# Kernel optimization log

Hardware: AMD Instinct MI355X
Metric: run time of the kernel (lower is better)

The kernel has to match this reference:

```python
import jax, jax.numpy as jnp
import numpy as np

D = 64          # embedding_dim
NU = 100000     # num_users
NI = 50000      # num_items
N = NU + NI     # total nodes
B = 16384       # batch of (user,item) pairs
CF = 256        # content_feat_dim
E = 2000000     # interaction edges (self loops added in forward)


def setup_inputs() -> dict:
    key = jax.random.key(0)
    ks = jax.random.split(key, 20)
    s = 0.05
    return {
        "user_ids": jnp.arange(B, dtype=jnp.int32),
        "item_ids": jnp.arange(B, dtype=jnp.int32),
        "content_features": jax.random.normal(ks[0], (B, CF), jnp.float32),
        "edge_index": jax.random.randint(ks[1], (2, E), 0, N, jnp.int32),
        # embeddings / projections
        "user_emb_w": jax.random.normal(ks[2], (NU, D), jnp.float32) * s,
        "item_emb_w": jax.random.normal(ks[3], (NI, D), jnp.float32) * s,
        "cp_w": jax.random.normal(ks[4], (CF, D), jnp.float32) * s,
        "cp_b": jnp.zeros((D,), jnp.float32),
        # GATConv1: in 2D, out D, heads 2, concat -> out dim 2D
        "w1": jax.random.normal(ks[5], (2 * D, 2 * D), jnp.float32) * s,
        "asrc1": jax.random.normal(ks[6], (2, D), jnp.float32) * s,
        "adst1": jax.random.normal(ks[7], (2, D), jnp.float32) * s,
        "b1": jnp.zeros((2 * D,), jnp.float32),
        # GATConv2: in 2D, out D, heads 1
        "w2": jax.random.normal(ks[8], (2 * D, D), jnp.float32) * s,
        "asrc2": jax.random.normal(ks[9], (1, D), jnp.float32) * s,
        "adst2": jax.random.normal(ks[10], (1, D), jnp.float32) * s,
        "b2": jnp.zeros((D,), jnp.float32),
        # predict head: Linear(3D,D) -> ReLU -> Linear(D,1)
        "pw1": jax.random.normal(ks[11], (3 * D, D), jnp.float32) * s,
        "pb1": jnp.zeros((D,), jnp.float32),
        "pw2": jax.random.normal(ks[12], (D, 1), jnp.float32) * s,
        "pb2": jnp.zeros((1,), jnp.float32),
    }


def _gat(x, src, dst, W, a_src, a_dst, bias, heads, C):
    # x: [N, in]; W: [in, heads*C]; a_src/a_dst: [heads, C]
    xw = (x @ W).reshape(N, heads, C)                      # [N,H,C]
    al_s = (xw * a_src[None]).sum(-1)                      # [N,H]
    al_d = (xw * a_dst[None]).sum(-1)                      # [N,H]
    e = jax.nn.leaky_relu(al_s[src] + al_d[dst], 0.2)      # [Et,H]
    m = jax.ops.segment_max(e, dst, num_segments=N)        # segment softmax
    ex = jnp.exp(e - m[dst])
    den = jax.ops.segment_sum(ex, dst, num_segments=N)
    alpha = ex / (den[dst] + 1e-16)                        # [Et,H]
    msg = xw[src] * alpha[:, :, None]                      # [Et,H,C]
    out = jax.ops.segment_sum(msg, dst, num_segments=N)    # [N,H,C]
    return out.reshape(N, heads * C) + bias


def reference(user_ids, item_ids, content_features, edge_index,
              user_emb_w, item_emb_w, cp_w, cp_b,
              w1, asrc1, adst1, b1, w2, asrc2, adst2, b2,
              pw1, pb1, pw2, pb2):
    u_emb = user_emb_w[user_ids]                           # [B,D]
    i_emb = item_emb_w[item_ids]                           # [B,D]
    c_emb = content_features @ cp_w + cp_b                 # [B,D]

    x = jnp.zeros((N, 2 * D), dtype=u_emb.dtype)
    x = x.at[user_ids].set(jnp.concatenate([u_emb, jnp.zeros_like(c_emb)], 1))
    x = x.at[NU + item_ids].set(jnp.concatenate([i_emb, c_emb], 1))

    loop = jnp.arange(N, dtype=edge_index.dtype)           # add_self_loops
    src = jnp.concatenate([edge_index[0], loop])
    dst = jnp.concatenate([edge_index[1], loop])

    x = jax.nn.elu(_gat(x, src, dst, w1, asrc1, adst1, b1, 2, D))  # [N,2D]
    x = _gat(x, src, dst, w2, asrc2, adst2, b2, 1, D)              # [N,D]

    combined = jnp.concatenate([u_emb, x[NU + item_ids], x[user_ids]], 1)  # [B,3D]
    h = jax.nn.relu(combined @ pw1 + pb1)
    return (h @ pw2 + pb2).squeeze(-1)                     # [B]
```

## Files before the change

### kernel.cpp

```cpp
#include <hip/hip_runtime.h>
#include <hip/hip_fp16.h>
#include <math.h>

static constexpr int ND  = 150000;
static constexpr int NUU = 100000;
static constexpr int BB  = 16384;
static constexpr int EE  = 2000000;
static constexpr int ETOT = EE + ND;
static constexpr int MACT = 2 * BB;

static constexpr int NBUK  = (ND + 127) >> 7;
static constexpr int CAP   = 4096;
static constexpr int CHUNK = 4096;
static constexpr int NCH   = (ETOT + CHUNK - 1) / CHUNK;
static constexpr int NBMW  = (ND + 31) / 32;
static constexpr unsigned long long M21 = 0x1FFFFF;

typedef _Float16 h8 __attribute__((ext_vector_type(8)));
typedef float    f4 __attribute__((ext_vector_type(4)));

__device__ __forceinline__ float wsum64(float v){
#pragma unroll
  for (int d = 32; d > 0; d >>= 1) v += __shfl_xor(v, d, 64);
  return v;
}

__global__ __launch_bounds__(256) void k_prep(const float* __restrict__ content,
    const float* __restrict__ cpw, const float* __restrict__ cpb,
    float* __restrict__ cemb,
    const float* __restrict__ w1, const float* __restrict__ w2,
    __half* __restrict__ Wt1, __half* __restrict__ Wt2,
    const float* __restrict__ asrc1, const float* __restrict__ adst1,
    const float* __restrict__ asrc2, const float* __restrict__ adst2,
    float* __restrict__ wa1s, float* __restrict__ wa1d,
    float* __restrict__ wa2s, float* __restrict__ wa2d){
  __shared__ __align__(16) float As[64 * 68];
  __shared__ __align__(16) float Ws[64 * 68];
  int tid = threadIdx.x;
  if (blockIdx.x < 256) {
    int m_base = blockIdx.x * 64;
    int tm = (tid >> 4) * 4, tn = (tid & 15) * 4;
    int lm = tid >> 2, lq = tid & 3;
    float acc[4][4];
#pragma unroll
    for (int i = 0; i < 4; i++)
#pragma unroll
      for (int j = 0; j < 4; j++) acc[i][j] = 0.f;
    for (int ks = 0; ks < 256; ks += 64) {
#pragma unroll
      for (int p = 0; p < 4; p++) {
        float4 v = *(const float4*)(content + (size_t)(m_base + lm) * 256 + ks + lq * 16 + p * 4);
        *(float4*)(As + lm * 68 + lq * 16 + p * 4) = v;
      }
#pragma unroll
      for (int p = 0; p < 4; p++) {
        int n4 = lq + p * 4;
        float4 v = *(const float4*)(cpw + (size_t)(ks + lm) * 64 + n4 * 4);
        *(float4*)(Ws + lm * 68 + n4 * 4) = v;
      }
      __syncthreads();
#pragma unroll
      for (int kk = 0; kk < 64; kk += 4) {
        float4 a[4], wv[4];
#pragma unroll
        for (int i = 0; i < 4; i++) a[i] = *(const float4*)(As + (tm + i) * 68 + kk);
#pragma unroll
        for (int q = 0; q < 4; q++) wv[q] = *(const float4*)(Ws + (kk + q) * 68 + tn);
#pragma unroll
        for (int i = 0; i < 4; i++) {
          acc[i][0] = fmaf(a[i].x, wv[0].x, acc[i][0]); acc[i][1] = fmaf(a[i].x, wv[0].y, acc[i][1]);
          acc[i][2] = fmaf(a[i].x, wv[0].z, acc[i][2]); acc[i][3] = fmaf(a[i].x, wv[0].w, acc[i][3]);
          acc[i][0] = fmaf(a[i].y, wv[1].x, acc[i][0]); acc[i][1] = fmaf(a[i].y, wv[1].y, acc[i][1]);
          acc[i][2] = fmaf(a[i].y, wv[1].z, acc[i][2]); acc[i][3] = fmaf(a[i].y, wv[1].w, acc[i][3]);
          acc[i][0] = fmaf(a[i].z, wv[2].x, acc[i][0]); acc[i][1] = fmaf(a[i].z, wv[2].y, acc[i][1]);
          acc[i][2] = fmaf(a[i].z, wv[2].z, acc[i][2]); acc[i][3] = fmaf(a[i].z, wv[2].w, acc[i][3]);
          acc[i][0] = fmaf(a[i].w, wv[3].x, acc[i][0]); acc[i][1] = fmaf(a[i].w, wv[3].y, acc[i][1]);
          acc[i][2] = fmaf(a[i].w, wv[3].z, acc[i][2]); acc[i][3] = fmaf(a[i].w, wv[3].w, acc[i][3]);
        }
      }
      __syncthreads();
    }
    float4 bias = *(const float4*)(cpb + tn);
#pragma unroll
    for (int i = 0; i < 4; i++) {
      float4 o = make_float4(acc[i][0] + bias.x, acc[i][1] + bias.y,
                             acc[i][2] + bias.z, acc[i][3] + bias.w);
      *(float4*)(cemb + (size_t)(m_base + tm + i) * 64 + tn) = o;
    }
  } else if (blockIdx.x < 352) {
    int t = (blockIdx.x - 256) * 256 + tid;
    if (t < 16384) {
      int n = t >> 7, k = t & 127;
      Wt1[t] = __float2half(w1[k * 128 + n]);
    } else {
      int u = t - 16384;
      int n = u >> 7, k = u & 127;
      Wt2[u] = __float2half(w2[k * 64 + n]);
    }
  } else if (tid < 128) {
    int k = tid;
    float s0 = 0.f, s1 = 0.f, d0 = 0.f, d1 = 0.f, s2 = 0.f, d2 = 0.f;
    for (int c = 0; c < 64; c++) {
      float wA = w1[k * 128 + c];
      float wB = w1[k * 128 + 64 + c];
      s0 = fmaf(wA, asrc1[c], s0);       d0 = fmaf(wA, adst1[c], d0);
      s1 = fmaf(wB, asrc1[64 + c], s1);  d1 = fmaf(wB, adst1[64 + c], d1);
      float wC = w2[k * 64 + c];
      s2 = fmaf(wC, asrc2[c], s2);       d2 = fmaf(wC, adst2[c], d2);
    }
    wa1s[k * 2] = s0; wa1s[k * 2 + 1] = s1;
    wa1d[k * 2] = d0; wa1d[k * 2 + 1] = d1;
    wa2s[k] = s2; wa2d[k] = d2;
  }
}

__global__ __launch_bounds__(256) void k_scatter(const int* __restrict__ uids,
    const float* __restrict__ uemb, const float* __restrict__ cemb,
    const float* __restrict__ iemb, const int* __restrict__ iids,
    __half* __restrict__ xc,
    const float* __restrict__ wa1s, const float* __restrict__ wa1d,
    float* __restrict__ als1c, float* __restrict__ ald1,
    int* __restrict__ flags, unsigned* __restrict__ bitmap,
    int* __restrict__ nodeOfC){
  int t = blockIdx.x * 256 + threadIdx.x;
  int r = t >> 6, c = t & 63;
  float2 ws = *(const float2*)(wa1s + 2 * c);
  float2 wd = *(const float2*)(wa1d + 2 * c);
  if (r < BB) {
    int uid = uids[r];
    float u = uemb[(size_t)uid * 64 + c];
    xc[(size_t)r * 128 + c]      = __float2half(u);
    xc[(size_t)r * 128 + 64 + c] = __float2half(0.f);
    float s0 = wsum64(u * ws.x);
    float s1 = wsum64(u * ws.y);
    float d0 = wsum64(u * wd.x);
    float d1 = wsum64(u * wd.y);
    if (c == 0) {
      *(float2*)(als1c + (size_t)r * 2) = make_float2(s0, s1);
      *(float2*)(ald1 + (size_t)uid * 2) = make_float2(d0, d1);
      flags[uid] = r;
      nodeOfC[r] = uid;
      atomicOr(&bitmap[uid >> 5], 1u << (uid & 31));
    }
  } else {
    int b = r - BB;
    int iid = iids[b];
    int node = NUU + iid;
    float lo = iemb[(size_t)iid * 64 + c];
    float hi = cemb[(size_t)b * 64 + c];
    xc[(size_t)r * 128 + c]      = __float2half(lo);
    xc[(size_t)r * 128 + 64 + c] = __float2half(hi);
    float2 wsH = *(const float2*)(wa1s + 128 + 2 * c);
    float2 wdH = *(const float2*)(wa1d + 128 + 2 * c);
    float s0 = wsum64(lo * ws.x + hi * wsH.x);
    float s1 = wsum64(lo * ws.y + hi * wsH.y);
    float d0 = wsum64(lo * wd.x + hi * wdH.x);
    float d1 = wsum64(lo * wd.y + hi * wdH.y);
    if (c == 0) {
      *(float2*)(als1c + (size_t)r * 2) = make_float2(s0, s1);
      *(float2*)(ald1 + (size_t)node * 2) = make_float2(d0, d1);
      flags[node] = r;
      nodeOfC[r] = node;
      atomicOr(&bitmap[node >> 5], 1u << (node & 31));
    }
  }
}

__global__ __launch_bounds__(256) void k_bin(const int* __restrict__ ei,
    const unsigned* __restrict__ bitmap, unsigned long long* __restrict__ bcnt64,
    int* __restrict__ bdata){
  __shared__ unsigned long long h64[NBUK];
  __shared__ int base[NBUK];
  __shared__ int hist[NBUK];
  int tid = threadIdx.x;
  int t0 = blockIdx.x * CHUNK;
  for (int i = tid; i < NBUK; i += 256) h64[i] = 0ull;
  __syncthreads();
  for (int i = tid; i < CHUNK; i += 256) {
    int t = t0 + i;
    if (t >= ETOT) break;
    int src, dst;
    if (t < EE) { src = ei[t]; dst = ei[EE + t]; }
    else        { src = dst = t - EE; }
    unsigned long long sa = (bitmap[src >> 5] >> (src & 31)) & 1;
    unsigned long long da = (bitmap[dst >> 5] >> (dst & 31)) & 1;
    atomicAdd(&h64[dst >> 7], 1ull | (sa << 21) | (da << 42));
  }
  __syncthreads();
  for (int b = tid; b < NBUK; b += 256) {
    unsigned long long v = h64[b];
    base[b] = v ? (int)(atomicAdd(&bcnt64[b], v) & M21) : 0;
    hist[b] = 0;
  }
  __syncthreads();
  for (int i = tid; i < CHUNK; i += 256) {
    int t = t0 + i;
    if (t >= ETOT) break;
    int src, dst;
    if (t < EE) { src = ei[t]; dst = ei[EE + t]; }
    else        { src = dst = t - EE; }
    int sa = (bitmap[src >> 5] >> (src & 31)) & 1;
    int da = (bitmap[dst >> 5] >> (dst & 31)) & 1;
    int b = dst >> 7;
    int r = base[b] + atomicAdd(&hist[b], 1);
    if (r < CAP)
      bdata[(size_t)b * CAP + r] = src | (sa << 18) | (da << 19) | ((dst & 127) << 20);
  }
}

__global__ void k_bscan(const unsigned long long* __restrict__ bcnt64,
    int* __restrict__ bbaseA, int* __restrict__ bbaseB,
    int* __restrict__ offsA_end, int* __restrict__ csrA, int* __restrict__ csrB){
  int lane = threadIdx.x;
  int cA = 0, cB = 0;
  for (int c0 = 0; c0 < NBUK; c0 += 64) {
    int i = c0 + lane;
    unsigned long long v = (i < NBUK) ? bcnt64[i] : 0ull;
    int a = (int)((v >> 21) & M21);
    int b = (int)((v >> 42) & M21);
    int xa = a, xb = b;
#pragma unroll
    for (int d = 1; d < 64; d <<= 1) {
      int ta = __shfl_up(xa, d, 64); if (lane >= d) xa += ta;
      int tb = __shfl_up(xb, d, 64); if (lane >= d) xb += tb;
    }
    if (i < NBUK) { bbaseA[i] = cA + xa - a; bbaseB[i] = cB + xb - b; }
    cA += __shfl(xa, 63, 64);
    cB += __shfl(xb, 63, 64);
  }
  if (lane == 0) *offsA_end = cA;
  if (lane < 16) { csrA[cA + lane] = 0; csrB[cB + lane] = 0; }
}

__global__ __launch_bounds__(256) void k_bucket(const int* __restrict__ bdata,
    const unsigned long long* __restrict__ bcnt64,
    const int* __restrict__ bbaseA, const int* __restrict__ bbaseB,
    const int* __restrict__ flags,
    int* __restrict__ offsA, int* __restrict__ inactA,
    int* __restrict__ startB, int* __restrict__ degBv,
    int* __restrict__ csrA, int* __restrict__ csrB){
  __shared__ int degAll[128], degAct[128], curA[128], curB[128];
  int b = blockIdx.x;
  int tid = threadIdx.x;
  int cnt = (int)(bcnt64[b] & M21);
  const int* bd = bdata + (size_t)b * CAP;
  if (tid < 128) { degAll[tid] = 0; degAct[tid] = 0; }
  __syncthreads();
  for (int i = tid; i < cnt; i += 256) {
    int e = bd[i];
    int d7 = (e >> 20) & 127;
    atomicAdd(&degAll[d7], 1);
    if ((e >> 18) & 1) atomicAdd(&degAct[d7], 1);
  }
  __syncthreads();
  if (tid < 64) {
    int g0 = b * 128 + tid, g1 = g0 + 64;
    int A0 = degAll[tid], A1 = degAll[64 + tid];
    int a0 = degAct[tid], a1 = degAct[64 + tid];
    int s0 = a0, s1 = a1;
#pragma unroll
    for (int d = 1; d < 64; d <<= 1) {
      int t0 = __shfl_up(s0, d, 64); if (tid >= d) s0 += t0;
      int t1 = __shfl_up(s1, d, 64); if (tid >= d) s1 += t1;
    }
    int totA0 = __shfl(s0, 63, 64);
    int eA0 = s0 - a0, eA1 = s1 - a1 + totA0;
    int baseA = bbaseA[b];
    curA[tid] = baseA + eA0; curA[64 + tid] = baseA + eA1;
    if (g0 < ND) { offsA[g0] = baseA + eA0; inactA[g0] = A0 - a0; }
    if (g1 < ND) { offsA[g1] = baseA + eA1; inactA[g1] = A1 - a1; }
    int f0 = (g0 < ND) ? flags[g0] : -1;
    int f1 = (g1 < ND) ? flags[g1] : -1;
    int w0 = (f0 >= 0) ? A0 : 0, w1 = (f1 >= 0) ? A1 : 0;
    int t0 = w0, t1 = w1;
#pragma unroll
    for (int d = 1; d < 64; d <<= 1) {
      int u0 = __shfl_up(t0, d, 64); if (tid >= d) t0 += u0;
      int u1 = __shfl_up(t1, d, 64); if (tid >= d) t1 += u1;
    }
    int totB0 = __shfl(t0, 63, 64);
    int eB0 = t0 - w0, eB1 = t1 - w1 + totB0;
    int baseB = bbaseB[b];
    curB[tid] = baseB + eB0; curB[64 + tid] = baseB + eB1;
    if (f0 >= 0) { startB[f0] = baseB + eB0; degBv[f0] = A0; }
    if (f1 >= 0) { startB[f1] = baseB + eB1; degBv[f1] = A1; }
  }
  __syncthreads();
  for (int i = tid; i < cnt; i += 256) {
    int e = bd[i];
    int d7 = (e >> 20) & 127;
    int src = e & 0x3FFFF;
    if ((e >> 19) & 1) { int p = atomicAdd(&curB[d7], 1); csrB[p] = src; }
    if ((e >> 18) & 1) {
      int ci = flags[src];
      int p = atomicAdd(&curA[d7], 1);
      csrA[p] = ci;
    }
  }
}

template<int NT>
__global__ __launch_bounds__(256) void k_mfma(const __half* __restrict__ A,
    const __half* __restrict__ Bt, __half* __restrict__ C, int M){
  constexpr int N = NT * 16;
  int wid  = (blockIdx.x * 256 + threadIdx.x) >> 6;
  int lane = threadIdx.x & 63;
  int q = lane >> 4, mr = lane & 15;
  int r0 = wid * 32;
  if (r0 >= M) return;
  int row0 = min(r0 + mr, M - 1);
  int row1 = min(r0 + 16 + mr, M - 1);
  f4 acc[2][NT];
#pragma unroll
  for (int i = 0; i < 2; i++)
#pragma unroll
    for (int j = 0; j < NT; j++) acc[i][j] = (f4)0.f;
#pragma unroll
  for (int ks = 0; ks < 4; ks++) {
    int ko = ks * 32 + q * 8;
    h8 a0 = *(const h8*)(A + (size_t)row0 * 128 + ko);
    h8 a1 = *(const h8*)(A + (size_t)row1 * 128 + ko);
#pragma unroll
    for (int nt = 0; nt < NT; nt++) {
      h8 b = *(const h8*)(Bt + (size_t)(nt * 16 + mr) * 128 + ko);
      acc[0][nt] = __builtin_amdgcn_mfma_f32_16x16x32_f16(a0, b, acc[0][nt], 0, 0, 0);
      acc[1][nt] = __builtin_amdgcn_mfma_f32_16x16x32_f16(a1, b, acc[1][nt], 0, 0, 0);
    }
  }
#pragma unroll
  for (int mt = 0; mt < 2; mt++)
#pragma unroll
    for (int r = 0; r < 4; r++) {
      int row = r0 + mt * 16 + q * 4 + r;
      if (row < M) {
#pragma unroll
        for (int nt = 0; nt < NT; nt++)
          C[(size_t)row * N + nt * 16 + mr] = __float2half(acc[mt][nt][r]);
      }
    }
}

template<int U>
__device__ __forceinline__ void gat2_blk(const int* __restrict__ cp, int j0,
    const float* __restrict__ myp, const __half2* __restrict__ xw, int lane,
    float& accx, float& accy){
  __half2 hv[U]; float pj[U];
#pragma unroll
  for (int u = 0; u < U; u++) {
    int sj = __builtin_amdgcn_readfirstlane(cp[j0 + u]);
    hv[u] = xw[(size_t)sj * 64 + lane];
    pj[u] = myp[j0 + u];
  }
#pragma unroll
  for (int u = 0; u < U; u++) {
    float2 fv = __half22float2(hv[u]);
    accx = fmaf(pj[u], fv.x, accx);
    accy = fmaf(pj[u], fv.y, accy);
  }
}

template<int U>
__device__ __forceinline__ void gat1_blk(const int* __restrict__ cp, int j0,
    const float* __restrict__ myp, const __half2* __restrict__ xw, int cw, int hid,
    float& accx, float& accy){
  __half2 hv[U]; float pj[U];
#pragma unroll
  for (int u = 0; u < U; u++) {
    int j = j0 + 2 * u;
    int s0 = __builtin_amdgcn_readfirstlane(cp[j]);
    int s1 = __builtin_amdgcn_readfirstlane(cp[j + 1]);
    int sel = hid ? s1 : s0;
    hv[u] = xw[(size_t)sel * 32 + cw];
    pj[u] = myp[j];
  }
#pragma unroll
  for (int u = 0; u < U; u++) {
    float2 fv = __half22float2(hv[u]);
    accx = fmaf(pj[u], fv.x, accx);
    accy = fmaf(pj[u], fv.y, accy);
  }
}

__global__ __launch_bounds__(256) void k_agg2(const __half2* __restrict__ xwc,
    const float* __restrict__ als1c, const float* __restrict__ ald1,
    const int* __restrict__ offsA, const int* __restrict__ inactA,
    const int* __restrict__ csrA,
    const float* __restrict__ bias, __half* __restrict__ out,
    const float* __restrict__ wa2s, const float* __restrict__ wa2d,
    float* __restrict__ als2, float* __restrict__ ald2, int n){
  __shared__ float pshare[4][2][64];
  int gw = (blockIdx.x * 256 + threadIdx.x) >> 6;
  int lane = threadIdx.x & 63;
  int ws = (threadIdx.x >> 6) & 3;
  if (gw >= n) return;
  int e0 = __builtin_amdgcn_readfirstlane(offsA[gw]);
  int e1 = __builtin_amdgcn_readfirstlane(offsA[gw + 1]);
  int inact = __builtin_amdgcn_readfirstlane(inactA[gw]);
  float2 aldv = *(const float2*)(ald1 + (size_t)gw * 2);
  bool lo = lane < 32;
  const float* myp = &pshare[ws][0][0] + (lo ? 0 : 64);
  float den0 = 0.f, den1 = 0.f, accx = 0.f, accy = 0.f;
  for (int base = e0; base < e1; base += 64) {
    int e = base + lane;
    bool valid = (e < e1);
    int srcv = valid ? csrA[e] : 0;
    float p0 = 0.f, p1 = 0.f;
    if (valid) {
      float2 a = *(const float2*)(als1c + (size_t)srcv * 2);
      float v0 = a.x + aldv.x, v1 = a.y + aldv.y;
      v0 = fmaxf(v0, 0.2f * v0);
      v1 = fmaxf(v1, 0.2f * v1);
      p0 = __expf(v0); p1 = __expf(v1);
    }
    den0 += p0; den1 += p1;
    pshare[ws][0][lane] = p0;
    pshare[ws][1][lane] = p1;
    int cnt = min(e1 - base, 64);
    const int* cp = csrA + base;
    int j = 0;
    for (; j + 16 <= cnt; j += 16) gat2_blk<16>(cp, j, myp, xwc, lane, accx, accy);
    if (j + 8 <= cnt) { gat2_blk<8>(cp, j, myp, xwc, lane, accx, accy); j += 8; }
    if (j + 4 <= cnt) { gat2_blk<4>(cp, j, myp, xwc, lane, accx, accy); j += 4; }
    if (j + 2 <= cnt) { gat2_blk<2>(cp, j, myp, xwc, lane, accx, accy); j += 2; }
    if (j < cnt)        gat2_blk<1>(cp, j, myp, xwc, lane, accx, accy);
  }
  float pin0 = __expf(fmaxf(aldv.x, 0.2f * aldv.x));
  float pin1 = __expf(fmaxf(aldv.y, 0.2f * aldv.y));
  float dt0 = wsum64(den0) + (float)inact * pin0;
  float dt1 = wsum64(den1) + (float)inact * pin1;
  float den = (lo ? dt0 : dt1) + 1e-16f;
  float inv = 1.f / den;
  float2 b = *(const float2*)(bias + 2 * lane);
  float vx = accx * inv + b.x;
  float vy = accy * inv + b.y;
  vx = (vx > 0.f) ? vx : expm1f(vx);
  vy = (vy > 0.f) ? vy : expm1f(vy);
  *(__half2*)(out + (size_t)gw * 128 + 2 * lane) = __floats2half2_rn(vx, vy);
  float2 wsv = *(const float2*)(wa2s + 2 * lane);
  float2 wdv = *(const float2*)(wa2d + 2 * lane);
  float s_s = wsum64(vx * wsv.x + vy * wsv.y);
  float s_d = wsum64(vx * wdv.x + vy * wdv.y);
  if (lane == 0) { als2[gw] = s_s; ald2[gw] = s_d; }
}

__global__ __launch_bounds__(256) void k_agg1(const __half2* __restrict__ xw2,
    const float* __restrict__ als2, const float* __restrict__ ald2,
    const int* __restrict__ startB, const int* __restrict__ degBv,
    const int* __restrict__ nodeOfC, const int* __restrict__ csrB,
    const float* __restrict__ bias, __half* __restrict__ out2c, int n){
  __shared__ float pshare[4][64];
  int c = (blockIdx.x * 256 + threadIdx.x) >> 6;
  int lane = threadIdx.x & 63;
  int ws = (threadIdx.x >> 6) & 3;
  if (c >= n) return;
  int e0  = __builtin_amdgcn_readfirstlane(startB[c]);
  int deg = __builtin_amdgcn_readfirstlane(degBv[c]);
  int e1 = e0 + deg;
  int dst = nodeOfC[c];
  float aldd = ald2[dst];
  int hid = lane >> 5;
  int cw = lane & 31;
  const float* myp = &pshare[ws][0] + hid;
  float den = 0.f, accx = 0.f, accy = 0.f;
  for (int base = e0; base < e1; base += 64) {
    int e = base + lane;
    bool valid = (e < e1);
    int srcv = valid ? csrB[e] : 0;
    float p = 0.f;
    if (valid) {
      float v = als2[srcv] + aldd;
      v = fmaxf(v, 0.2f * v);
      p = __expf(v);
    }
    den += p;
    pshare[ws][lane] = p;
    int cnt = min(e1 - base, 64);
    const int* cp = csrB + base;
    int j = 0;
    for (; j + 16 <= cnt; j += 16) gat1_blk<8>(cp, j, myp, xw2, cw, hid, accx, accy);
    if (j + 8 <= cnt) { gat1_blk<4>(cp, j, myp, xw2, cw, hid, accx, accy); j += 8; }
    if (j + 4 <= cnt) { gat1_blk<2>(cp, j, myp, xw2, cw, hid, accx, accy); j += 4; }
    for (; j < cnt; j += 2) gat1_blk<1>(cp, j, myp, xw2, cw, hid, accx, accy);
  }
  accx += __shfl_xor(accx, 32, 64);
  accy += __shfl_xor(accy, 32, 64);
  float dent = wsum64(den);
  if (lane < 32) {
    float inv = 1.f / (dent + 1e-16f);
    float2 b = *(const float2*)(bias + 2 * cw);
    float vx = accx * inv + b.x;
    float vy = accy * inv + b.y;
    *(__half2*)(out2c + (size_t)c * 64 + 2 * cw) = __floats2half2_rn(vx, vy);
  }
}

__global__ __launch_bounds__(256) void k_head(const float* __restrict__ uemb,
    const int* __restrict__ uids,
    const __half* __restrict__ out2c, const float* __restrict__ pw1,
    const float* __restrict__ pb1, const float* __restrict__ pw2,
    const float* __restrict__ pb2, float* __restrict__ out, int B){
  __shared__ __align__(16) float As[64][196];
  __shared__ __align__(16) float Ws[192][64];
  int tid = threadIdx.x;
  for (int i = tid; i < 192 * 64 / 4; i += 256)
    ((float4*)&Ws[0][0])[i] = ((const float4*)pw1)[i];
  int w = tid >> 6, lane = tid & 63;
  int rbase = blockIdx.x * 64;
  for (int r = w; r < 64; r += 4) {
    int b = rbase + r;
    int uid = uids[b];
    As[r][lane]       = uemb[(size_t)uid * 64 + lane];
    As[r][64 + lane]  = __half2float(out2c[(size_t)(BB + b) * 64 + lane]);
    As[r][128 + lane] = __half2float(out2c[(size_t)b * 64 + lane]);
  }
  __syncthreads();
  int tm = (tid >> 4) * 4;
  int tn = (tid & 15) * 4;
  float acc[4][4];
#pragma unroll
  for (int i = 0; i < 4; i++)
#pragma unroll
    for (int j = 0; j < 4; j++) acc[i][j] = 0.f;
  for (int k = 0; k < 192; k += 4) {
    float4 a[4], wv[4];
#pragma unroll
    for (int i = 0; i < 4; i++) a[i] = *(const float4*)&As[tm + i][k];
#pragma unroll
    for (int q = 0; q < 4; q++) wv[q] = *(const float4*)&Ws[k + q][tn];
#pragma unroll
    for (int i = 0; i < 4; i++) {
      acc[i][0] = fmaf(a[i].x, wv[0].x, acc[i][0]); acc[i][1] = fmaf(a[i].x, wv[0].y, acc[i][1]);
      acc[i][2] = fmaf(a[i].x, wv[0].z, acc[i][2]); acc[i][3] = fmaf(a[i].x, wv[0].w, acc[i][3]);
      acc[i][0] = fmaf(a[i].y, wv[1].x, acc[i][0]); acc[i][1] = fmaf(a[i].y, wv[1].y, acc[i][1]);
      acc[i][2] = fmaf(a[i].y, wv[1].z, acc[i][2]); acc[i][3] = fmaf(a[i].y, wv[1].w, acc[i][3]);
      acc[i][0] = fmaf(a[i].z, wv[2].x, acc[i][0]); acc[i][1] = fmaf(a[i].z, wv[2].y, acc[i][1]);
      acc[i][2] = fmaf(a[i].z, wv[2].z, acc[i][2]); acc[i][3] = fmaf(a[i].z, wv[2].w, acc[i][3]);
      acc[i][0] = fmaf(a[i].w, wv[3].x, acc[i][0]); acc[i][1] = fmaf(a[i].w, wv[3].y, acc[i][1]);
      acc[i][2] = fmaf(a[i].w, wv[3].z, acc[i][2]); acc[i][3] = fmaf(a[i].w, wv[3].w, acc[i][3]);
    }
  }
  float4 pb1v = *(const float4*)(pb1 + tn);
  float4 pw2v = *(const float4*)(pw2 + tn);
  float pb2v = pb2[0];
#pragma unroll
  for (int i = 0; i < 4; i++) {
    float h0 = fmaxf(acc[i][0] + pb1v.x, 0.f);
    float h1 = fmaxf(acc[i][1] + pb1v.y, 0.f);
    float h2 = fmaxf(acc[i][2] + pb1v.z, 0.f);
    float h3 = fmaxf(acc[i][3] + pb1v.w, 0.f);
    float part = h0 * pw2v.x + h1 * pw2v.y + h2 * pw2v.z + h3 * pw2v.w;
#pragma unroll
    for (int d = 1; d < 16; d <<= 1) part += __shfl_xor(part, d, 64);
    if ((tid & 15) == 0) out[rbase + tm + i] = part + pb2v;
  }
}

extern "C" void kernel_launch(void* const* d_in, const int* in_sizes, int n_in,
                              void* d_out, int out_size, void* d_ws, size_t ws_size,
                              hipStream_t stream) {
  (void)in_sizes; (void)n_in; (void)out_size; (void)ws_size;
  const int*   user_ids = (const int*)  d_in[0];
  const int*   item_ids = (const int*)  d_in[1];
  const float* content  = (const float*)d_in[2];
  const int*   edge_idx = (const int*)  d_in[3];
  const float* uemb     = (const float*)d_in[4];
  const float* iemb     = (const float*)d_in[5];
  const float* cp_w     = (const float*)d_in[6];
  const float* cp_b     = (const float*)d_in[7];
  const float* w1       = (const float*)d_in[8];
  const float* asrc1    = (const float*)d_in[9];
  const float* adst1    = (const float*)d_in[10];
  const float* b1       = (const float*)d_in[11];
  const float* w2       = (const float*)d_in[12];
  const float* asrc2    = (const float*)d_in[13];
  const float* adst2    = (const float*)d_in[14];
  const float* b2       = (const float*)d_in[15];
  const float* pw1      = (const float*)d_in[16];
  const float* pb1      = (const float*)d_in[17];
  const float* pw2      = (const float*)d_in[18];
  const float* pb2      = (const float*)d_in[19];
  float* out = (float*)d_out;

  char* p = (char*)d_ws;
  int*    bdata = (int*)p;
  __half* x1    = (__half*)p;
  p += (size_t)ND * 128 * 2;
  __half* xc   = (__half*)p; p += (size_t)MACT * 128 * 2;
  __half* xwc  = (__half*)p; p += (size_t)MACT * 128 * 2;
  __half* xw2  = (__half*)p; p += (size_t)ND * 64 * 2;
  __half* out2c= (__half*)p; p += (size_t)MACT * 64 * 2;
  float* cemb  = (float*)p;  p += (size_t)BB * 64 * 4;
  __half* Wt1  = (__half*)p; p += 16384 * 2;
  __half* Wt2  = (__half*)p; p += 8192 * 2;
  float* ald1     = (float*)p;
  unsigned* bitmap= (unsigned*)(ald1 + (size_t)ND * 2);
  unsigned long long* bcnt64 = (unsigned long long*)(bitmap + NBMW);
  size_t zbytes   = (char*)(bcnt64 + NBUK) - (char*)ald1;
  p = (char*)(bcnt64 + NBUK);
  float* als1c = (float*)p; p += (size_t)MACT * 2 * 4;
  float* als2  = (float*)p; p += (size_t)ND * 4;
  float* ald2  = (float*)p; p += (size_t)ND * 4;
  int* flags   = (int*)p;   p += (size_t)ND * 4;
  int* nodeOfC = (int*)p;   p += (size_t)MACT * 4;
  int* inactA  = (int*)p;   p += (size_t)ND * 4;
  int* offsA   = (int*)p;   p += (size_t)(ND + 16) * 4;
  int* startB  = (int*)p;   p += (size_t)MACT * 4;
  int* degBv   = (int*)p;   p += (size_t)MACT * 4;
  int* bbaseA  = (int*)p;   p += NBUK * 4;
  int* bbaseB  = (int*)p;   p += NBUK * 4;
  int* csrA    = (int*)p;   p += (size_t)(ETOT + 16) * 4;
  int* csrB    = (int*)p;   p += (size_t)(ETOT + 16) * 4;
  float* wa1s  = (float*)p; p += 256 * 4;
  float* wa1d  = (float*)p; p += 256 * 4;
  float* wa2s  = (float*)p; p += 128 * 4;
  float* wa2d  = (float*)p; p += 128 * 4;

  hipMemsetAsync(flags, 0xFF, (size_t)ND * 4, stream);
  hipMemsetAsync(ald1, 0, zbytes, stream);

  k_prep<<<353, 256, 0, stream>>>(content, cp_w, cp_b, cemb, w1, w2, Wt1, Wt2,
                                  asrc1, adst1, asrc2, adst2,
                                  wa1s, wa1d, wa2s, wa2d);

  k_scatter<<<MACT * 64 / 256, 256, 0, stream>>>(user_ids, uemb, cemb, iemb, item_ids,
      xc, wa1s, wa1d, als1c, ald1, flags, bitmap, nodeOfC);

  k_bin<<<NCH, 256, 0, stream>>>(edge_idx, bitmap, bcnt64, bdata);
  k_bscan<<<1, 64, 0, stream>>>(bcnt64, bbaseA, bbaseB, offsA + ND, csrA, csrB);
  k_bucket<<<NBUK, 256, 0, stream>>>(bdata, bcnt64, bbaseA, bbaseB, flags,
                                     offsA, inactA, startB, degBv, csrA, csrB);

  k_mfma<8><<<(MACT + 127) / 128, 256, 0, stream>>>(xc, Wt1, xwc, MACT);
  k_agg2<<<((size_t)ND * 64 + 255) / 256, 256, 0, stream>>>((const __half2*)xwc,
      als1c, ald1, offsA, inactA, csrA, b1, x1, wa2s, wa2d, als2, ald2, ND);

  k_mfma<4><<<(ND + 127) / 128, 256, 0, stream>>>(x1, Wt2, xw2, ND);
  k_agg1<<<(MACT * 64) / 256, 256, 0, stream>>>((const __half2*)xw2, als2, ald2,
      startB, degBv, nodeOfC, csrB, b2, out2c, MACT);

  k_head<<<BB / 64, 256, 0, stream>>>(uemb, user_ids, out2c,
                                      pw1, pb1, pw2, pb2, out, BB);
}
```

Baseline: 376.4 us.

## Fold memsets into prep kernel, single-pass binning, 16-lane-per-node layer-1 aggregation

Result: faster. 323.2 us (-14.1%).

```diff
diff --git a/kernel.cpp b/kernel.cpp
--- a/kernel.cpp
+++ b/kernel.cpp
@@ -15,6 +15,9 @@
 static constexpr int NCH   = (ETOT + CHUNK - 1) / CHUNK;
 static constexpr int NBMW  = (ND + 31) / 32;
 static constexpr unsigned long long M21 = 0x1FFFFF;
+
+static constexpr int ZU4 = (ND * 8 + NBMW * 4 + NBUK * 8) / 16;
+static constexpr int FU4 = ND * 4 / 16;
 
 typedef _Float16 h8 __attribute__((ext_vector_type(8)));
 typedef float    f4 __attribute__((ext_vector_type(4)));
@@ -33,7 +36,8 @@
     const float* __restrict__ asrc1, const float* __restrict__ adst1,
     const float* __restrict__ asrc2, const float* __restrict__ adst2,
     float* __restrict__ wa1s, float* __restrict__ wa1d,
-    float* __restrict__ wa2s, float* __restrict__ wa2d){
+    float* __restrict__ wa2s, float* __restrict__ wa2d,
+    uint4* __restrict__ zbase, uint4* __restrict__ fbase){
   __shared__ __align__(16) float As[64 * 68];
   __shared__ __align__(16) float Ws[64 * 68];
   int tid = threadIdx.x;
@@ -97,20 +101,28 @@
       int n = u >> 7, k = u & 127;
       Wt2[u] = __float2half(w2[k * 64 + n]);
     }
-  } else if (tid < 128) {
-    int k = tid;
-    float s0 = 0.f, s1 = 0.f, d0 = 0.f, d1 = 0.f, s2 = 0.f, d2 = 0.f;
-    for (int c = 0; c < 64; c++) {
-      float wA = w1[k * 128 + c];
-      float wB = w1[k * 128 + 64 + c];
-      s0 = fmaf(wA, asrc1[c], s0);       d0 = fmaf(wA, adst1[c], d0);
-      s1 = fmaf(wB, asrc1[64 + c], s1);  d1 = fmaf(wB, adst1[64 + c], d1);
-      float wC = w2[k * 64 + c];
-      s2 = fmaf(wC, asrc2[c], s2);       d2 = fmaf(wC, adst2[c], d2);
-    }
-    wa1s[k * 2] = s0; wa1s[k * 2 + 1] = s1;
-    wa1d[k * 2] = d0; wa1d[k * 2 + 1] = d1;
-    wa2s[k] = s2; wa2d[k] = d2;
+  } else if (blockIdx.x == 352) {
+    if (tid < 128) {
+      int k = tid;
+      float s0 = 0.f, s1 = 0.f, d0 = 0.f, d1 = 0.f, s2 = 0.f, d2 = 0.f;
+      for (int c = 0; c < 64; c++) {
+        float wA = w1[k * 128 + c];
+        float wB = w1[k * 128 + 64 + c];
+        s0 = fmaf(wA, asrc1[c], s0);       d0 = fmaf(wA, adst1[c], d0);
+        s1 = fmaf(wB, asrc1[64 + c], s1);  d1 = fmaf(wB, adst1[64 + c], d1);
+        float wC = w2[k * 64 + c];
+        s2 = fmaf(wC, asrc2[c], s2);       d2 = fmaf(wC, adst2[c], d2);
+      }
+      wa1s[k * 2] = s0; wa1s[k * 2 + 1] = s1;
+      wa1d[k * 2] = d0; wa1d[k * 2 + 1] = d1;
+      wa2s[k] = s2; wa2d[k] = d2;
+    }
+  } else if (blockIdx.x < 393) {
+    uint4 zv = make_uint4(0, 0, 0, 0);
+    for (int i = (blockIdx.x - 353) * 256 + tid; i < ZU4; i += 40 * 256) zbase[i] = zv;
+  } else {
+    uint4 fv = make_uint4(~0u, ~0u, ~0u, ~0u);
+    for (int i = (blockIdx.x - 393) * 256 + tid; i < FU4; i += 16 * 256) fbase[i] = fv;
   }
 }
 
@@ -170,41 +182,40 @@
     const unsigned* __restrict__ bitmap, unsigned long long* __restrict__ bcnt64,
     int* __restrict__ bdata){
   __shared__ unsigned long long h64[NBUK];
-  __shared__ int base[NBUK];
-  __shared__ int hist[NBUK];
+  __shared__ int sbase[NBUK];
   int tid = threadIdx.x;
   int t0 = blockIdx.x * CHUNK;
   for (int i = tid; i < NBUK; i += 256) h64[i] = 0ull;
   __syncthreads();
-  for (int i = tid; i < CHUNK; i += 256) {
-    int t = t0 + i;
-    if (t >= ETOT) break;
-    int src, dst;
-    if (t < EE) { src = ei[t]; dst = ei[EE + t]; }
-    else        { src = dst = t - EE; }
-    unsigned long long sa = (bitmap[src >> 5] >> (src & 31)) & 1;
-    unsigned long long da = (bitmap[dst >> 5] >> (dst & 31)) & 1;
-    atomicAdd(&h64[dst >> 7], 1ull | (sa << 21) | (da << 42));
+  int epk[16], rb[16];
+#pragma unroll
+  for (int i = 0; i < 16; i++) {
+    int t = t0 + i * 256 + tid;
+    if (t < ETOT) {
+      int src, dst;
+      if (t < EE) { src = ei[t]; dst = ei[EE + t]; }
+      else        { src = dst = t - EE; }
+      unsigned long long sa = (bitmap[src >> 5] >> (src & 31)) & 1;
+      unsigned long long da = (bitmap[dst >> 5] >> (dst & 31)) & 1;
+      int b = dst >> 7;
+      unsigned long long ret = atomicAdd(&h64[b], 1ull | (sa << 21) | (da << 42));
+      epk[i] = src | ((int)sa << 18) | ((int)da << 19) | ((dst & 127) << 20);
+      rb[i] = (b << 12) | (int)(ret & 0xFFF);
+    } else rb[i] = -1;
   }
   __syncthreads();
   for (int b = tid; b < NBUK; b += 256) {
     unsigned long long v = h64[b];
-    base[b] = v ? (int)(atomicAdd(&bcnt64[b], v) & M21) : 0;
-    hist[b] = 0;
+    sbase[b] = v ? (int)(atomicAdd(&bcnt64[b], v) & M21) : 0;
   }
   __syncthreads();
-  for (int i = tid; i < CHUNK; i += 256) {
-    int t = t0 + i;
-    if (t >= ETOT) break;
-    int src, dst;
-    if (t < EE) { src = ei[t]; dst = ei[EE + t]; }
-    else        { src = dst = t - EE; }
-    int sa = (bitmap[src >> 5] >> (src & 31)) & 1;
-    int da = (bitmap[dst >> 5] >> (dst & 31)) & 1;
-    int b = dst >> 7;
-    int r = base[b] + atomicAdd(&hist[b], 1);
-    if (r < CAP)
-      bdata[(size_t)b * CAP + r] = src | (sa << 18) | (da << 19) | ((dst & 127) << 20);
+#pragma unroll
+  for (int i = 0; i < 16; i++) {
+    if (rb[i] >= 0) {
+      int b = rb[i] >> 12;
+      int r = sbase[b] + (rb[i] & 0xFFF);
+      if (r < CAP) bdata[(size_t)b * CAP + r] = epk[i];
+    }
   }
 }
 
@@ -239,24 +250,25 @@
     int* __restrict__ offsA, int* __restrict__ inactA,
     int* __restrict__ startB, int* __restrict__ degBv,
     int* __restrict__ csrA, int* __restrict__ csrB){
-  __shared__ int degAll[128], degAct[128], curA[128], curB[128];
+  __shared__ int deg2[128], curA[128], curB[128];
   int b = blockIdx.x;
   int tid = threadIdx.x;
   int cnt = (int)(bcnt64[b] & M21);
+  if (cnt > CAP) cnt = CAP;
   const int* bd = bdata + (size_t)b * CAP;
-  if (tid < 128) { degAll[tid] = 0; degAct[tid] = 0; }
+  if (tid < 128) deg2[tid] = 0;
   __syncthreads();
   for (int i = tid; i < cnt; i += 256) {
     int e = bd[i];
     int d7 = (e >> 20) & 127;
-    atomicAdd(&degAll[d7], 1);
-    if ((e >> 18) & 1) atomicAdd(&degAct[d7], 1);
+    atomicAdd(&deg2[d7], 1 + (((e >> 18) & 1) << 16));
   }
   __syncthreads();
   if (tid < 64) {
     int g0 = b * 128 + tid, g1 = g0 + 64;
-    int A0 = degAll[tid], A1 = degAll[64 + tid];
-    int a0 = degAct[tid], a1 = degAct[64 + tid];
+    int v0 = deg2[tid], v1 = deg2[64 + tid];
+    int A0 = v0 & 0xFFFF, A1 = v1 & 0xFFFF;
+    int a0 = v0 >> 16,    a1 = v1 >> 16;
     int s0 = a0, s1 = a1;
 #pragma unroll
     for (int d = 1; d < 64; d <<= 1) {
@@ -340,68 +352,31 @@
     }
 }
 
-template<int U>
-__device__ __forceinline__ void gat2_blk(const int* __restrict__ cp, int j0,
-    const float* __restrict__ myp, const __half2* __restrict__ xw, int lane,
-    float& accx, float& accy){
-  __half2 hv[U]; float pj[U];
-#pragma unroll
-  for (int u = 0; u < U; u++) {
-    int sj = __builtin_amdgcn_readfirstlane(cp[j0 + u]);
-    hv[u] = xw[(size_t)sj * 64 + lane];
-    pj[u] = myp[j0 + u];
-  }
-#pragma unroll
-  for (int u = 0; u < U; u++) {
-    float2 fv = __half22float2(hv[u]);
-    accx = fmaf(pj[u], fv.x, accx);
-    accy = fmaf(pj[u], fv.y, accy);
-  }
-}
-
-template<int U>
-__device__ __forceinline__ void gat1_blk(const int* __restrict__ cp, int j0,
-    const float* __restrict__ myp, const __half2* __restrict__ xw, int cw, int hid,
-    float& accx, float& accy){
-  __half2 hv[U]; float pj[U];
-#pragma unroll
-  for (int u = 0; u < U; u++) {
-    int j = j0 + 2 * u;
-    int s0 = __builtin_amdgcn_readfirstlane(cp[j]);
-    int s1 = __builtin_amdgcn_readfirstlane(cp[j + 1]);
-    int sel = hid ? s1 : s0;
-    hv[u] = xw[(size_t)sel * 32 + cw];
-    pj[u] = myp[j];
-  }
-#pragma unroll
-  for (int u = 0; u < U; u++) {
-    float2 fv = __half22float2(hv[u]);
-    accx = fmaf(pj[u], fv.x, accx);
-    accy = fmaf(pj[u], fv.y, accy);
-  }
-}
-
-__global__ __launch_bounds__(256) void k_agg2(const __half2* __restrict__ xwc,
+__global__ __launch_bounds__(256) void k_agg2(const __half* __restrict__ xwc,
     const float* __restrict__ als1c, const float* __restrict__ ald1,
     const int* __restrict__ offsA, const int* __restrict__ inactA,
     const int* __restrict__ csrA,
     const float* __restrict__ bias, __half* __restrict__ out,
     const float* __restrict__ wa2s, const float* __restrict__ wa2d,
     float* __restrict__ als2, float* __restrict__ ald2, int n){
-  __shared__ float pshare[4][2][64];
-  int gw = (blockIdx.x * 256 + threadIdx.x) >> 6;
   int lane = threadIdx.x & 63;
-  int ws = (threadIdx.x >> 6) & 3;
-  if (gw >= n) return;
-  int e0 = __builtin_amdgcn_readfirstlane(offsA[gw]);
-  int e1 = __builtin_amdgcn_readfirstlane(offsA[gw + 1]);
-  int inact = __builtin_amdgcn_readfirstlane(inactA[gw]);
-  float2 aldv = *(const float2*)(ald1 + (size_t)gw * 2);
-  bool lo = lane < 32;
-  const float* myp = &pshare[ws][0][0] + (lo ? 0 : 64);
-  float den0 = 0.f, den1 = 0.f, accx = 0.f, accy = 0.f;
-  for (int base = e0; base < e1; base += 64) {
-    int e = base + lane;
+  int gl   = lane & 15;
+  int gbase = lane & 48;
+  int w4   = (blockIdx.x * 256 + threadIdx.x) >> 6;
+  int dst  = w4 * 4 + (lane >> 4);
+  if (dst >= n) return;
+  int e0 = offsA[dst];
+  int e1 = offsA[dst + 1];
+  int inact = inactA[dst];
+  float2 aldv = *(const float2*)(ald1 + (size_t)dst * 2);
+  bool headlo = (gl < 8);
+  float den0 = 0.f, den1 = 0.f;
+  float acc[8];
+#pragma unroll
+  for (int k = 0; k < 8; k++) acc[k] = 0.f;
+  const uint4* xr = (const uint4*)xwc;
+  for (int base = e0; base < e1; base += 16) {
+    int e = base + gl;
     bool valid = (e < e1);
     int srcv = valid ? csrA[e] : 0;
     float p0 = 0.f, p1 = 0.f;
@@ -413,34 +388,83 @@
       p0 = __expf(v0); p1 = __expf(v1);
     }
     den0 += p0; den1 += p1;
-    pshare[ws][0][lane] = p0;
-    pshare[ws][1][lane] = p1;
-    int cnt = min(e1 - base, 64);
-    const int* cp = csrA + base;
-    int j = 0;
-    for (; j + 16 <= cnt; j += 16) gat2_blk<16>(cp, j, myp, xwc, lane, accx, accy);
-    if (j + 8 <= cnt) { gat2_blk<8>(cp, j, myp, xwc, lane, accx, accy); j += 8; }
-    if (j + 4 <= cnt) { gat2_blk<4>(cp, j, myp, xwc, lane, accx, accy); j += 4; }
-    if (j + 2 <= cnt) { gat2_blk<2>(cp, j, myp, xwc, lane, accx, accy); j += 2; }
-    if (j < cnt)        gat2_blk<1>(cp, j, myp, xwc, lane, accx, accy);
+    int cnt = min(e1 - base, 16);
+    for (int j = 0; j < cnt; j++) {
+      int li = gbase + j;
+      int sj = __shfl(srcv, li, 64);
+      float q0 = __shfl(p0, li, 64);
+      float q1 = __shfl(p1, li, 64);
+      float pj = headlo ? q0 : q1;
+      union { uint4 u; __half2 h[4]; } hv;
+      hv.u = xr[(size_t)sj * 16 + gl];
+#pragma unroll
+      for (int k = 0; k < 4; k++) {
+        float2 fv = __half22float2(hv.h[k]);
+        acc[2*k]   = fmaf(pj, fv.x, acc[2*k]);
+        acc[2*k+1] = fmaf(pj, fv.y, acc[2*k+1]);
+      }
+    }
+  }
+#pragma unroll
+  for (int d = 1; d < 16; d <<= 1) {
+    den0 += __shfl_xor(den0, d, 64);
+    den1 += __shfl_xor(den1, d, 64);
   }
   float pin0 = __expf(fmaxf(aldv.x, 0.2f * aldv.x));
   float pin1 = __expf(fmaxf(aldv.y, 0.2f * aldv.y));
-  float dt0 = wsum64(den0) + (float)inact * pin0;
-  float dt1 = wsum64(den1) + (float)inact * pin1;
-  float den = (lo ? dt0 : dt1) + 1e-16f;
-  float inv = 1.f / den;
-  float2 b = *(const float2*)(bias + 2 * lane);
-  float vx = accx * inv + b.x;
-  float vy = accy * inv + b.y;
-  vx = (vx > 0.f) ? vx : expm1f(vx);
-  vy = (vy > 0.f) ? vy : expm1f(vy);
-  *(__half2*)(out + (size_t)gw * 128 + 2 * lane) = __floats2half2_rn(vx, vy);
-  float2 wsv = *(const float2*)(wa2s + 2 * lane);
-  float2 wdv = *(const float2*)(wa2d + 2 * lane);
-  float s_s = wsum64(vx * wsv.x + vy * wsv.y);
-  float s_d = wsum64(vx * wdv.x + vy * wdv.y);
-  if (lane == 0) { als2[gw] = s_s; ald2[gw] = s_d; }
+  float dt0 = den0 + (float)inact * pin0;
+  float dt1 = den1 + (float)inact * pin1;
+  float den = (headlo ? dt0 : dt1) + 1e-16f;
+  float inv = __builtin_amdgcn_rcpf(den);
+  float4 b0 = *(const float4*)(bias + 8 * gl);
+  float4 b1 = *(const float4*)(bias + 8 * gl + 4);
+  float v[8];
+  v[0] = acc[0]*inv + b0.x; v[1] = acc[1]*inv + b0.y;
+  v[2] = acc[2]*inv + b0.z; v[3] = acc[3]*inv + b0.w;
+  v[4] = acc[4]*inv + b1.x; v[5] = acc[5]*inv + b1.y;
+  v[6] = acc[6]*inv + b1.z; v[7] = acc[7]*inv + b1.w;
+#pragma unroll
+  for (int k = 0; k < 8; k++) v[k] = (v[k] > 0.f) ? v[k] : (__expf(v[k]) - 1.f);
+  union { uint4 u; __half2 h[4]; } ov;
+#pragma unroll
+  for (int k = 0; k < 4; k++) ov.h[k] = __floats2half2_rn(v[2*k], v[2*k+1]);
+  *(uint4*)(out + (size_t)dst * 128 + 8 * gl) = ov.u;
+  float4 ws0 = *(const float4*)(wa2s + 8 * gl);
+  float4 ws1 = *(const float4*)(wa2s + 8 * gl + 4);
+  float4 wd0 = *(const float4*)(wa2d + 8 * gl);
+  float4 wd1 = *(const float4*)(wa2d + 8 * gl + 4);
+  float ss = v[0]*ws0.x + v[1]*ws0.y + v[2]*ws0.z + v[3]*ws0.w
+           + v[4]*ws1.x + v[5]*ws1.y + v[6]*ws1.z + v[7]*ws1.w;
+  float sd = v[0]*wd0.x + v[1]*wd0.y + v[2]*wd0.z + v[3]*wd0.w
+           + v[4]*wd1.x + v[5]*wd1.y + v[6]*wd1.z + v[7]*wd1.w;
+#pragma unroll
+  for (int d = 1; d < 16; d <<= 1) {
+    ss += __shfl_xor(ss, d, 64);
+    sd += __shfl_xor(sd, d, 64);
+  }
+  if (gl == 0) { als2[dst] = ss; ald2[dst] = sd; }
+}
+
+template<int U>
+__device__ __forceinline__ void gat1_blk(const int* __restrict__ cp, int j0,
+    const float* __restrict__ myp, const __half2* __restrict__ xw, int cw, int hid,
+    float& accx, float& accy){
+  __half2 hv[U]; float pj[U];
+#pragma unroll
+  for (int u = 0; u < U; u++) {
+    int j = j0 + 2 * u;
+    int s0 = __builtin_amdgcn_readfirstlane(cp[j]);
+    int s1 = __builtin_amdgcn_readfirstlane(cp[j + 1]);
+    int sel = hid ? s1 : s0;
+    hv[u] = xw[(size_t)sel * 32 + cw];
+    pj[u] = myp[j];
+  }
+#pragma unroll
+  for (int u = 0; u < U; u++) {
+    float2 fv = __half22float2(hv[u]);
+    accx = fmaf(pj[u], fv.x, accx);
+    accy = fmaf(pj[u], fv.y, accy);
+  }
 }
 
 __global__ __launch_bounds__(256) void k_agg1(const __half2* __restrict__ xw2,
@@ -486,7 +510,7 @@
   accy += __shfl_xor(accy, 32, 64);
   float dent = wsum64(den);
   if (lane < 32) {
-    float inv = 1.f / (dent + 1e-16f);
+    float inv = __builtin_amdgcn_rcpf(dent + 1e-16f);
     float2 b = *(const float2*)(bias + 2 * cw);
     float vx = accx * inv + b.x;
     float vy = accy * inv + b.y;
@@ -595,7 +619,6 @@
   float* ald1     = (float*)p;
   unsigned* bitmap= (unsigned*)(ald1 + (size_t)ND * 2);
   unsigned long long* bcnt64 = (unsigned long long*)(bitmap + NBMW);
-  size_t zbytes   = (char*)(bcnt64 + NBUK) - (char*)ald1;
   p = (char*)(bcnt64 + NBUK);
   float* als1c = (float*)p; p += (size_t)MACT * 2 * 4;
   float* als2  = (float*)p; p += (size_t)ND * 4;
@@ -615,12 +638,10 @@
   float* wa2s  = (float*)p; p += 128 * 4;
   float* wa2d  = (float*)p; p += 128 * 4;
 
-  hipMemsetAsync(flags, 0xFF, (size_t)ND * 4, stream);
-  hipMemsetAsync(ald1, 0, zbytes, stream);
-
-  k_prep<<<353, 256, 0, stream>>>(content, cp_w, cp_b, cemb, w1, w2, Wt1, Wt2,
+  k_prep<<<409, 256, 0, stream>>>(content, cp_w, cp_b, cemb, w1, w2, Wt1, Wt2,
                                   asrc1, adst1, asrc2, adst2,
-                                  wa1s, wa1d, wa2s, wa2d);
+                                  wa1s, wa1d, wa2s, wa2d,
+                                  (uint4*)ald1, (uint4*)flags);
 
   k_scatter<<<MACT * 64 / 256, 256, 0, stream>>>(user_ids, uemb, cemb, iemb, item_ids,
       xc, wa1s, wa1d, als1c, ald1, flags, bitmap, nodeOfC);
@@ -631,7 +652,7 @@
                                      offsA, inactA, startB, degBv, csrA, csrB);
 
   k_mfma<8><<<(MACT + 127) / 128, 256, 0, stream>>>(xc, Wt1, xwc, MACT);
-  k_agg2<<<((size_t)ND * 64 + 255) / 256, 256, 0, stream>>>((const __half2*)xwc,
+  k_agg2<<<(ND * 16 + 255) / 256, 256, 0, stream>>>(xwc,
       als1c, ald1, offsA, inactA, csrA, b1, x1, wa2s, wa2d, als2, ald2, ND);
 
   k_mfma<4><<<(ND + 127) / 128, 256, 0, stream>>>(x1, Wt2, xw2, ND);
```
